# Performance work log

Measured on AMD Instinct MI355X. Metric: run time of the kernel, lower is better.

The kernel has to match this reference:

```python
import jax, jax.numpy as jnp
import numpy as np

C0 = 32        # num_feat_maps[0]
LD = 6         # latent_dim
NC = 1         # num_classes
B, P = 1, 96


def setup_inputs() -> dict:
    key = jax.random.key(0)
    ks = jax.random.split(key, 10)
    s = lambda fan_in: 1.0 / np.sqrt(fan_in)
    return {
        "feature_map": jax.random.normal(ks[0], (B, C0, P, P, P), dtype=jnp.float32),
        "z": jax.random.normal(ks[1], (B, LD), dtype=jnp.float32),
        "w1": jax.random.normal(ks[2], (C0, C0 + LD), dtype=jnp.float32) * s(C0 + LD),
        "b1": jnp.zeros((C0,), dtype=jnp.float32),
        "w2": jax.random.normal(ks[3], (C0, C0), dtype=jnp.float32) * s(C0),
        "b2": jnp.zeros((C0,), dtype=jnp.float32),
        "w3": jax.random.normal(ks[4], (C0, C0), dtype=jnp.float32) * s(C0),
        "b3": jnp.zeros((C0,), dtype=jnp.float32),
        "wl": jax.random.normal(ks[5], (NC, C0), dtype=jnp.float32) * s(C0),
        "bl": jnp.zeros((NC,), dtype=jnp.float32),
    }


def _pw(x, w, b):
    # 1x1x1 conv3d == pointwise channel GEMM: [B,Ci,X,Y,Z] x [Co,Ci] -> [B,Co,X,Y,Z]
    return jnp.einsum('bcxyz,oc->boxyz', x, w) + b[None, :, None, None, None]


def reference(feature_map, z, w1, b1, w2, b2, w3, b3, wl, bl):
    b, _, x_, y_, z_ = feature_map.shape
    # tile() on the unsqueezed z is equivalent to broadcasting over spatial dims
    zb = jnp.broadcast_to(z[:, :, None, None, None], (b, z.shape[1], x_, y_, z_))
    h = jnp.concatenate([feature_map, zb], axis=1)          # [B, C0+LD, P,P,P]
    h = jax.nn.relu(_pw(h, w1, b1))
    h = jax.nn.relu(_pw(h, w2, b2))
    h = jax.nn.relu(_pw(h, w3, b3))
    return _pw(h, wl, bl)                                    # [B, NC, P,P,P]
```

## Files before the change

### kernel.cpp

```cpp
#include <hip/hip_runtime.h>


typedef float  f32x16 __attribute__((ext_vector_type(16)));
typedef short  bf16x8 __attribute__((ext_vector_type(8)));

constexpr int NPTS   = 96 * 96 * 96;
constexpr int NP2    = NPTS / 2;
constexpr int BLOCK  = 256;
constexpr int NBLK   = 864;
constexpr int GPW    = 4;

union FragU { unsigned u[4]; bf16x8 v; };

__device__ inline unsigned cvtpk(float lo, float hi) {
    unsigned d;
    asm("v_cvt_pk_bf16_f32 %0, %1, %2" : "=v"(d) : "v"(lo), "v"(hi));
    return d;
}
__device__ inline float unlo(unsigned d) { return __uint_as_float(d << 16); }
__device__ inline float unhi(unsigned d) { return __uint_as_float(d & 0xffff0000u); }

__device__ inline bf16x8 mk(unsigned d0, unsigned d1, unsigned d2, unsigned d3) {
    FragU f; f.u[0] = d0; f.u[1] = d1; f.u[2] = d2; f.u[3] = d3; return f.v;
}

__device__ inline void swap32(unsigned a, unsigned b, unsigned& x, unsigned& y) {
    auto r = __builtin_amdgcn_permlane32_swap(a, b, false, false);
    x = r[0]; y = r[1];
}

__device__ inline bf16x8 load_wfrag(const float* __restrict__ W, int stride,
                                    int row, int koff) {
    const float2* W2 = reinterpret_cast<const float2*>(W + row * stride + koff);
    float2 a = W2[0], b = W2[1], c = W2[2], d = W2[3];
    return mk(cvtpk(a.x, a.y), cvtpk(b.x, b.y), cvtpk(c.x, c.y), cvtpk(d.x, d.y));
}

__device__ inline void build_bfrags(const float* h,
                                    bf16x8& B0h, bf16x8& B0l,
                                    bf16x8& B1h, bf16x8& B1l) {
    unsigned hp[8], lp[8];
    #pragma unroll
    for (int j = 0; j < 8; ++j) {
        float h0 = fmaxf(h[2 * j], 0.f), h1 = fmaxf(h[2 * j + 1], 0.f);
        unsigned d = cvtpk(h0, h1);
        hp[j] = d;
        lp[j] = cvtpk(h0 - unlo(d), h1 - unhi(d));
    }
    unsigned a0, a1, b0, b1, c0, c1, d0, d1;
    swap32(hp[0], hp[2], a0, a1); swap32(hp[1], hp[3], b0, b1);
    swap32(hp[4], hp[6], c0, c1); swap32(hp[5], hp[7], d0, d1);
    B0h = mk(a0, b0, a1, b1);
    B1h = mk(c0, d0, c1, d1);
    swap32(lp[0], lp[2], a0, a1); swap32(lp[1], lp[3], b0, b1);
    swap32(lp[4], lp[6], c0, c1); swap32(lp[5], lp[7], d0, d1);
    B0l = mk(a0, b0, a1, b1);
    B1l = mk(c0, d0, c1, d1);
}

__global__ __launch_bounds__(BLOCK, 2)
void fused_mlp_mfma(const float* __restrict__ fm, const float* __restrict__ z,
                    const float* __restrict__ w1, const float* __restrict__ b1,
                    const float* __restrict__ w2, const float* __restrict__ b2,
                    const float* __restrict__ w3, const float* __restrict__ b3,
                    const float* __restrict__ wl, const float* __restrict__ bl,
                    float* __restrict__ out)
{
    const int lane = threadIdx.x & 63;
    const int wid  = blockIdx.x * (BLOCK / 64) + (threadIdx.x >> 6);
    const int hl   = lane >> 5;
    const int col  = lane & 31;
    const int koff = 8 * hl;

    bf16x8 W1f[2], W2f[2], W3f[2];
    #pragma unroll
    for (int h = 0; h < 2; ++h) {
        W1f[h] = load_wfrag(w1, 38, col, 16 * h + koff);
        W2f[h] = load_wfrag(w2, 32, col, 16 * h + koff);
        W3f[h] = load_wfrag(w3, 32, col, 16 * h + koff);
    }

    float zv[6];
    #pragma unroll
    for (int j = 0; j < 6; ++j) zv[j] = z[j];
    f32x16 B1f, B2f, B3f;
    float wlr[16];
    #pragma unroll
    for (int r = 0; r < 16; ++r) {
        const int ch = (r & 3) + 8 * (r >> 2) + 4 * hl;
        float t = b1[ch];
        #pragma unroll
        for (int j = 0; j < 6; ++j) t = fmaf(w1[ch * 38 + 32 + j], zv[j], t);
        B1f[r] = t;
        B2f[r] = b2[ch];
        B3f[r] = b3[ch];
        wlr[r] = wl[ch];
    }
    const float blv = bl[0];

    const float2* __restrict__ fm2 = reinterpret_cast<const float2*>(fm);
    float2* __restrict__ out2      = reinterpret_cast<float2*>(out);

    for (int it = 0; it < GPW; ++it) {
        const int g   = wid * GPW + it;
        const int pt2 = g * 32 + col;

        float2 v[16];
        #pragma unroll
        for (int i = 0; i < 16; ++i) {
            const int ch = ((i < 8) ? i : (8 + i)) + koff;
            v[i] = fm2[ch * NP2 + pt2];
        }

        f32x16 accE = B1f, accO = B1f;
        {
            unsigned he[8], le[8], ho[8], lo_[8];
            #pragma unroll
            for (int j = 0; j < 8; ++j) {
                float e0 = v[2 * j].x, e1 = v[2 * j + 1].x;
                unsigned d = cvtpk(e0, e1);
                he[j] = d; le[j] = cvtpk(e0 - unlo(d), e1 - unhi(d));
                float o0 = v[2 * j].y, o1 = v[2 * j + 1].y;
                unsigned q = cvtpk(o0, o1);
                ho[j] = q; lo_[j] = cvtpk(o0 - unlo(q), o1 - unhi(q));
            }
            accE = __builtin_amdgcn_mfma_f32_32x32x16_bf16(W1f[0], mk(he[0], he[1], he[2], he[3]), accE, 0, 0, 0);
            accE = __builtin_amdgcn_mfma_f32_32x32x16_bf16(W1f[0], mk(le[0], le[1], le[2], le[3]), accE, 0, 0, 0);
            accE = __builtin_amdgcn_mfma_f32_32x32x16_bf16(W1f[1], mk(he[4], he[5], he[6], he[7]), accE, 0, 0, 0);
            accE = __builtin_amdgcn_mfma_f32_32x32x16_bf16(W1f[1], mk(le[4], le[5], le[6], le[7]), accE, 0, 0, 0);
            accO = __builtin_amdgcn_mfma_f32_32x32x16_bf16(W1f[0], mk(ho[0], ho[1], ho[2], ho[3]), accO, 0, 0, 0);
            accO = __builtin_amdgcn_mfma_f32_32x32x16_bf16(W1f[0], mk(lo_[0], lo_[1], lo_[2], lo_[3]), accO, 0, 0, 0);
            accO = __builtin_amdgcn_mfma_f32_32x32x16_bf16(W1f[1], mk(ho[4], ho[5], ho[6], ho[7]), accO, 0, 0, 0);
            accO = __builtin_amdgcn_mfma_f32_32x32x16_bf16(W1f[1], mk(lo_[4], lo_[5], lo_[6], lo_[7]), accO, 0, 0, 0);
        }

        f32x16 nE, nO;
        {
            float hE[16], hO[16];
            #pragma unroll
            for (int r = 0; r < 16; ++r) { hE[r] = accE[r]; hO[r] = accO[r]; }
            bf16x8 E0h, E0l, E1h, E1l, O0h, O0l, O1h, O1l;
            build_bfrags(hE, E0h, E0l, E1h, E1l);
            build_bfrags(hO, O0h, O0l, O1h, O1l);
            nE = B2f; nO = B2f;
            nE = __builtin_amdgcn_mfma_f32_32x32x16_bf16(W2f[0], E0h, nE, 0, 0, 0);
            nE = __builtin_amdgcn_mfma_f32_32x32x16_bf16(W2f[0], E0l, nE, 0, 0, 0);
            nE = __builtin_amdgcn_mfma_f32_32x32x16_bf16(W2f[1], E1h, nE, 0, 0, 0);
            nE = __builtin_amdgcn_mfma_f32_32x32x16_bf16(W2f[1], E1l, nE, 0, 0, 0);
            nO = __builtin_amdgcn_mfma_f32_32x32x16_bf16(W2f[0], O0h, nO, 0, 0, 0);
            nO = __builtin_amdgcn_mfma_f32_32x32x16_bf16(W2f[0], O0l, nO, 0, 0, 0);
            nO = __builtin_amdgcn_mfma_f32_32x32x16_bf16(W2f[1], O1h, nO, 0, 0, 0);
            nO = __builtin_amdgcn_mfma_f32_32x32x16_bf16(W2f[1], O1l, nO, 0, 0, 0);
        }
        {
            float hE[16], hO[16];
            #pragma unroll
            for (int r = 0; r < 16; ++r) { hE[r] = nE[r]; hO[r] = nO[r]; }
            bf16x8 E0h, E0l, E1h, E1l, O0h, O0l, O1h, O1l;
            build_bfrags(hE, E0h, E0l, E1h, E1l);
            build_bfrags(hO, O0h, O0l, O1h, O1l);
            accE = B3f; accO = B3f;
            accE = __builtin_amdgcn_mfma_f32_32x32x16_bf16(W3f[0], E0h, accE, 0, 0, 0);
            accE = __builtin_amdgcn_mfma_f32_32x32x16_bf16(W3f[0], E0l, accE, 0, 0, 0);
            accE = __builtin_amdgcn_mfma_f32_32x32x16_bf16(W3f[1], E1h, accE, 0, 0, 0);
            accE = __builtin_amdgcn_mfma_f32_32x32x16_bf16(W3f[1], E1l, accE, 0, 0, 0);
            accO = __builtin_amdgcn_mfma_f32_32x32x16_bf16(W3f[0], O0h, accO, 0, 0, 0);
            accO = __builtin_amdgcn_mfma_f32_32x32x16_bf16(W3f[0], O0l, accO, 0, 0, 0);
            accO = __builtin_amdgcn_mfma_f32_32x32x16_bf16(W3f[1], O1h, accO, 0, 0, 0);
            accO = __builtin_amdgcn_mfma_f32_32x32x16_bf16(W3f[1], O1l, accO, 0, 0, 0);
        }

        float sE = 0.f, sO = 0.f;
        #pragma unroll
        for (int r = 0; r < 16; ++r) {
            sE = fmaf(wlr[r], fmaxf(accE[r], 0.f), sE);
            sO = fmaf(wlr[r], fmaxf(accO[r], 0.f), sO);
        }
        unsigned px, py;
        swap32(__float_as_uint(sE), __float_as_uint(sE), px, py);
        float totE = __uint_as_float(px) + __uint_as_float(py) + blv;
        swap32(__float_as_uint(sO), __float_as_uint(sO), px, py);
        float totO = __uint_as_float(px) + __uint_as_float(py) + blv;

        if (lane < 32) out2[pt2] = make_float2(totE, totO);
    }
}

extern "C" void kernel_launch(void* const* d_in, const int* in_sizes, int n_in,
                              void* d_out, int out_size, void* d_ws, size_t ws_size,
                              hipStream_t stream)
{
    const float* fm = (const float*)d_in[0];
    const float* z  = (const float*)d_in[1];
    const float* w1 = (const float*)d_in[2];
    const float* b1 = (const float*)d_in[3];
    const float* w2 = (const float*)d_in[4];
    const float* b2 = (const float*)d_in[5];
    const float* w3 = (const float*)d_in[6];
    const float* b3 = (const float*)d_in[7];
    const float* wl = (const float*)d_in[8];
    const float* bl = (const float*)d_in[9];
    float* out = (float*)d_out;

    fused_mlp_mfma<<<NBLK, BLOCK, 0, stream>>>(
        fm, z, w1, b1, w2, b2, w3, b3, wl, bl, out);
}
```

Baseline: 188.3 us.

## Prefetch both point groups up front and halve groups per wave

The per-wave group count drops from four to two and the block count doubles. Both groups' feature-map loads are issued at kernel start, before the weight and bias setup, so global-memory latency overlaps the setup work and the first group's compute. This gives more memory-level parallelism per wave and more waves in flight. The cost is higher register pressure from holding two sets of 32 floats, which may reduce occupancy under the existing launch bounds.

```diff
diff --git a/kernel.cpp b/kernel.cpp
--- a/kernel.cpp
+++ b/kernel.cpp
@@ -7,8 +7,8 @@
 constexpr int NPTS   = 96 * 96 * 96;
 constexpr int NP2    = NPTS / 2;
 constexpr int BLOCK  = 256;
-constexpr int NBLK   = 864;
-constexpr int GPW    = 4;
+constexpr int GPW    = 2;
+constexpr int NBLK   = 1728;
 
 union FragU { unsigned u[4]; bf16x8 v; };
 
@@ -72,6 +72,24 @@
     const int col  = lane & 31;
     const int koff = 8 * hl;
 
+    const float2* __restrict__ fm2 = reinterpret_cast<const float2*>(fm);
+    float2* __restrict__ out2      = reinterpret_cast<float2*>(out);
+
+    const int g0   = wid * GPW;
+    const int pt2a = (g0 + 0) * 32 + col;
+    const int pt2b = (g0 + 1) * 32 + col;
+    float2 va[16], vb[16];
+    #pragma unroll
+    for (int i = 0; i < 16; ++i) {
+        const int ch = ((i < 8) ? i : (8 + i)) + koff;
+        va[i] = fm2[ch * NP2 + pt2a];
+    }
+    #pragma unroll
+    for (int i = 0; i < 16; ++i) {
+        const int ch = ((i < 8) ? i : (8 + i)) + koff;
+        vb[i] = fm2[ch * NP2 + pt2b];
+    }
+
     bf16x8 W1f[2], W2f[2], W3f[2];
     #pragma unroll
     for (int h = 0; h < 2; ++h) {
@@ -98,20 +116,7 @@
     }
     const float blv = bl[0];
 
-    const float2* __restrict__ fm2 = reinterpret_cast<const float2*>(fm);
-    float2* __restrict__ out2      = reinterpret_cast<float2*>(out);
-
-    for (int it = 0; it < GPW; ++it) {
-        const int g   = wid * GPW + it;
-        const int pt2 = g * 32 + col;
-
-        float2 v[16];
-        #pragma unroll
-        for (int i = 0; i < 16; ++i) {
-            const int ch = ((i < 8) ? i : (8 + i)) + koff;
-            v[i] = fm2[ch * NP2 + pt2];
-        }
-
+    auto compute_group = [&](const float2* v, int pt2) {
         f32x16 accE = B1f, accO = B1f;
         {
             unsigned he[8], le[8], ho[8], lo_[8];
@@ -152,6 +157,7 @@
             nO = __builtin_amdgcn_mfma_f32_32x32x16_bf16(W2f[1], O1h, nO, 0, 0, 0);
             nO = __builtin_amdgcn_mfma_f32_32x32x16_bf16(W2f[1], O1l, nO, 0, 0, 0);
         }
+        f32x16 accE2, accO2;
         {
             float hE[16], hO[16];
             #pragma unroll
@@ -159,22 +165,22 @@
             bf16x8 E0h, E0l, E1h, E1l, O0h, O0l, O1h, O1l;
             build_bfrags(hE, E0h, E0l, E1h, E1l);
             build_bfrags(hO, O0h, O0l, O1h, O1l);
-            accE = B3f; accO = B3f;
-            accE = __builtin_amdgcn_mfma_f32_32x32x16_bf16(W3f[0], E0h, accE, 0, 0, 0);
-            accE = __builtin_amdgcn_mfma_f32_32x32x16_bf16(W3f[0], E0l, accE, 0, 0, 0);
-            accE = __builtin_amdgcn_mfma_f32_32x32x16_bf16(W3f[1], E1h, accE, 0, 0, 0);
-            accE = __builtin_amdgcn_mfma_f32_32x32x16_bf16(W3f[1], E1l, accE, 0, 0, 0);
-            accO = __builtin_amdgcn_mfma_f32_32x32x16_bf16(W3f[0], O0h, accO, 0, 0, 0);
-            accO = __builtin_amdgcn_mfma_f32_32x32x16_bf16(W3f[0], O0l, accO, 0, 0, 0);
-            accO = __builtin_amdgcn_mfma_f32_32x32x16_bf16(W3f[1], O1h, accO, 0, 0, 0);
-            accO = __builtin_amdgcn_mfma_f32_32x32x16_bf16(W3f[1], O1l, accO, 0, 0, 0);
+            accE2 = B3f; accO2 = B3f;
+            accE2 = __builtin_amdgcn_mfma_f32_32x32x16_bf16(W3f[0], E0h, accE2, 0, 0, 0);
+            accE2 = __builtin_amdgcn_mfma_f32_32x32x16_bf16(W3f[0], E0l, accE2, 0, 0, 0);
+            accE2 = __builtin_amdgcn_mfma_f32_32x32x16_bf16(W3f[1], E1h, accE2, 0, 0, 0);
+            accE2 = __builtin_amdgcn_mfma_f32_32x32x16_bf16(W3f[1], E1l, accE2, 0, 0, 0);
+            accO2 = __builtin_amdgcn_mfma_f32_32x32x16_bf16(W3f[0], O0h, accO2, 0, 0, 0);
+            accO2 = __builtin_amdgcn_mfma_f32_32x32x16_bf16(W3f[0], O0l, accO2, 0, 0, 0);
+            accO2 = __builtin_amdgcn_mfma_f32_32x32x16_bf16(W3f[1], O1h, accO2, 0, 0, 0);
+            accO2 = __builtin_amdgcn_mfma_f32_32x32x16_bf16(W3f[1], O1l, accO2, 0, 0, 0);
         }
 
         float sE = 0.f, sO = 0.f;
         #pragma unroll
         for (int r = 0; r < 16; ++r) {
-            sE = fmaf(wlr[r], fmaxf(accE[r], 0.f), sE);
-            sO = fmaf(wlr[r], fmaxf(accO[r], 0.f), sO);
+            sE = fmaf(wlr[r], fmaxf(accE2[r], 0.f), sE);
+            sO = fmaf(wlr[r], fmaxf(accO2[r], 0.f), sO);
         }
         unsigned px, py;
         swap32(__float_as_uint(sE), __float_as_uint(sE), px, py);
@@ -183,7 +189,10 @@
         float totO = __uint_as_float(px) + __uint_as_float(py) + blv;
 
         if (lane < 32) out2[pt2] = make_float2(totE, totO);
-    }
+    };
+
+    compute_group(va, pt2a);
+    compute_group(vb, pt2b);
 }
 
 extern "C" void kernel_launch(void* const* d_in, const int* in_sizes, int n_in,
```

New measurement: 192.2 us. 2.1% more time.
